# Kernel tuning notes

Measured on AMD Instinct MI355X. Metric: run time of the kernel, lower is better.

Reference implementation:

```python
import jax, jax.numpy as jnp
import numpy as np

DIM = 256
HEADS = 8
HD = DIM // HEADS  # 32
WS = 8             # window size
N = WS * WS        # 64 tokens per window
BN_SCALE = 1.0 / np.sqrt(1.0 + 1e-5)  # BatchNorm with default running stats (mean 0, var 1)


def _relative_position_index():
    # static int index table [N, N], computed with numpy (matches torch buffer)
    coords = np.stack(np.meshgrid(np.arange(WS), np.arange(WS), indexing='ij'))  # (2, ws, ws)
    cf = coords.reshape(2, -1)                                                   # (2, N)
    rel = cf[:, :, None] - cf[:, None, :]                                        # (2, N, N)
    rel = rel.transpose(1, 2, 0)                                                 # (N, N, 2)
    rel[:, :, 0] += WS - 1
    rel[:, :, 1] += WS - 1
    rel[:, :, 0] *= 2 * WS - 1
    return jnp.asarray(rel.sum(-1))  # (N, N)


def _relative_coords_table():
    # static float table [(2ws-1), (2ws-1), 2] with Swin-V2 log-spaced coords
    r = np.arange(-(WS - 1), WS, dtype=np.float32)
    g = np.stack(np.meshgrid(r, r, indexing='ij'), axis=-1)  # (L, L, 2)
    g = g / (WS - 1) * 8.0
    g = np.sign(g) * np.log2(np.abs(g) + 1.0) / np.log2(8.0)
    return jnp.asarray(g)


def setup_inputs() -> dict:
    key = jax.random.key(0)
    ks = jax.random.split(key, 9)
    B, H, W = 16, 64, 64
    s = 0.02
    return {
        'x': jax.random.normal(ks[0], (B, DIM, H, W), dtype=jnp.float32),
        'qkv_w': jax.random.normal(ks[1], (3 * DIM, DIM), dtype=jnp.float32) * s,
        'qkv_b': jax.random.normal(ks[2], (3 * DIM,), dtype=jnp.float32) * s,
        'proj_w': jax.random.normal(ks[3], (DIM, DIM), dtype=jnp.float32) * s,
        'proj_b': jax.random.normal(ks[4], (DIM,), dtype=jnp.float32) * s,
        'cpb_w1': jax.random.normal(ks[5], (DIM, 2), dtype=jnp.float32) * 0.5,
        'cpb_b1': jax.random.normal(ks[6], (DIM,), dtype=jnp.float32) * 0.5,
        'cpb_w2': jax.random.normal(ks[7], (HEADS, DIM), dtype=jnp.float32) * 0.1,
        'dw_w': jax.random.normal(ks[8], (DIM, 1, 7, 7), dtype=jnp.float32) * s,
    }


def reference(x, qkv_w, qkv_b, proj_w, proj_b, cpb_w1, cpb_b1, cpb_w2, dw_w):
    B, C, H, W = x.shape
    Hn, Wn = H // WS, W // WS
    B_ = B * Hn * Wn

    # continuous position bias: pointwise MLP (conv1x1+BN+SiLU, conv1x1+BN)
    tbl = _relative_coords_table()                          # (L, L, 2)
    h = jax.nn.silu((tbl @ cpb_w1.T + cpb_b1) * BN_SCALE)   # (L, L, DIM)
    bias_table = (h @ cpb_w2.T) * BN_SCALE                  # (L, L, HEADS)
    bias_table = bias_table.reshape(-1, HEADS)
    rpi = _relative_position_index()
    bias = bias_table[rpi.reshape(-1)].reshape(N, N, HEADS).transpose(2, 0, 1)
    bias = 16.0 * jax.nn.sigmoid(bias)                      # (HEADS, N, N)

    # qkv 1x1 conv, window partition
    qkv = jnp.einsum('oc,bchw->bohw', qkv_w, x) + qkv_b[None, :, None, None]
    win = qkv.reshape(B, 3 * C, Hn, WS, Wn, WS).transpose(0, 2, 4, 1, 3, 5)
    win = win.reshape(B_, 3 * C, N)
    qkvw = win.reshape(B_, 3, HEADS, HD, N).transpose(1, 0, 2, 4, 3)  # (3, B_, H, N, hd)
    q, k, v = qkvw[0], qkvw[1], qkvw[2]

    # SDPA with additive bias (attn_mask)
    scores = jnp.einsum('bhnd,bhmd->bhnm', q, k) / np.sqrt(HD) + bias[None]
    attn = jax.nn.softmax(scores, axis=-1)
    o = jnp.einsum('bhnm,bhmd->bhnd', attn, v)

    def window_reverse(w):  # (B_, N, C) -> (B, C, H, W)
        t = w.reshape(B, Hn, Wn, WS, WS, C).transpose(0, 5, 1, 3, 2, 4)
        return t.reshape(B, C, H, W)

    x_img = window_reverse(o.transpose(0, 2, 1, 3).reshape(B_, N, C))
    v_img = window_reverse(v.transpose(0, 2, 1, 3).reshape(B_, N, C))

    # depthwise 7x7 positional encoding on v, residual add
    pe = jax.lax.conv_general_dilated(
        v_img, dw_w, window_strides=(1, 1), padding='SAME',
        feature_group_count=C, dimension_numbers=('NCHW', 'OIHW', 'NCHW'))
    out = x_img + pe
    out = jnp.einsum('oc,bchw->bohw', proj_w, out) + proj_b[None, :, None, None]
    return out
```

## Files before the change

### kernel.cpp

```cpp
#include <hip/hip_runtime.h>
#include <cstdint>
#include <cstddef>

typedef unsigned short u16;
typedef unsigned int   u32;

#define LW     15
#define BNS    0.9999950000374997f
#define SCALE  0.17677669529663687f

typedef __bf16 bf16x8 __attribute__((ext_vector_type(8)));
typedef float  f32x4  __attribute__((ext_vector_type(4)));
typedef u16    u16x8  __attribute__((ext_vector_type(8)));

__device__ __forceinline__ u16 f2bf(float f){
  union { float f; u32 i; } v; v.f = f;
  u32 r = v.i + 0x7FFFu + ((v.i >> 16) & 1u);
  return (u16)(r >> 16);
}
__device__ __forceinline__ float bf2f(u16 u){
  union { u32 i; float f; } v; v.i = ((u32)u) << 16; return v.f;
}

__global__ void k_cvt_w(const float* __restrict__ qw, const float* __restrict__ pw,
                        u16* __restrict__ qwb, u16* __restrict__ pwb){
  const int i = blockIdx.x*256 + threadIdx.x;
  if (i < 196608) qwb[i] = f2bf(qw[i]);
  else            pwb[i - 196608] = f2bf(pw[i - 196608]);
}

__global__ void k_cpb_mlp(const float* __restrict__ w1, const float* __restrict__ b1,
                          const float* __restrict__ w2, float* __restrict__ tab){
  const int e = blockIdx.x;
  const int c = threadIdx.x;
  const float a0 = (float)(e / LW - 7);
  const float a1 = (float)(e % LW - 7);
  const float cx = copysignf(log2f(fabsf(a0)*(8.f/7.f) + 1.f) * (1.f/3.f), a0);
  const float cy = copysignf(log2f(fabsf(a1)*(8.f/7.f) + 1.f) * (1.f/3.f), a1);
  float pre = (cx*w1[2*c] + cy*w1[2*c+1] + b1[c]) * BNS;
  float hid = pre / (1.f + __expf(-pre));
  __shared__ float hl[256];
  hl[c] = hid;
  __syncthreads();
  if (c < 8){
    float s = 0.f;
    for (int i = 0; i < 256; ++i) s += hl[i] * w2[c*256 + i];
    tab[e*8 + c] = s * BNS;
  }
}

__global__ void k_bias_expand(const float* __restrict__ tab, float* __restrict__ biasQ){
  const int id = blockIdx.x*256 + threadIdx.x;
  const int key = id & 63;
  const int q   = (id >> 6) & 63;
  const int h   = id >> 12;
  const int dy = (q >> 3) - (key >> 3) + 7;
  const int dx = (q & 7)  - (key & 7)  + 7;
  const float v = tab[(dy*LW + dx)*8 + h];
  biasQ[id] = 16.f / (1.f + __expf(-v));
}

__global__ __launch_bounds__(512, 4) void k_qkv_attn(
    const float* __restrict__ x, const u16* __restrict__ qwb,
    const float* __restrict__ qb, const float* __restrict__ biasQ,
    float* __restrict__ xout, u16* __restrict__ vout){
  const int win = blockIdx.x;
  const int b = win >> 6, wy = (win >> 3) & 7, wx = win & 7;
  __shared__ __align__(16) char smem[70656];
  u16* xs = (u16*)smem;
  const int tid  = threadIdx.x;
  const int wave = tid >> 6, lane = tid & 63;
  const int quad = lane >> 4, l16 = lane & 15;
  u16* vbw = (u16*)(smem + 33792 + wave*4608);

  const float* xbase = x + (size_t)b*256*4096 + (size_t)(wy*8)*64 + wx*8;
  for (int i = tid; i < 4096; i += 512){
    const int c  = i >> 4;
    const int g  = i & 15;
    const int py = g >> 1, xh = (g & 1) * 4;
    float4 v4 = *(const float4*)&xbase[(size_t)c*4096 + py*64 + xh];
    const int n0 = py*8 + xh;
    xs[(n0+0)*264 + c] = f2bf(v4.x);
    xs[(n0+1)*264 + c] = f2bf(v4.y);
    xs[(n0+2)*264 + c] = f2bf(v4.z);
    xs[(n0+3)*264 + c] = f2bf(v4.w);
  }
  __syncthreads();

  const int h = wave;
  const f32x4 zero4 = {0.f, 0.f, 0.f, 0.f};

  auto run_gemm = [&](int sec, u32 (&w)[2][4][2]){
    f32x4 acc[2][4];
    #pragma unroll
    for (int rt = 0; rt < 2; ++rt)
      #pragma unroll
      for (int tt = 0; tt < 4; ++tt) acc[rt][tt] = zero4;
    #pragma unroll
    for (int kh2 = 0; kh2 < 2; ++kh2){
      bf16x8 af[2][4];
      #pragma unroll
      for (int rt = 0; rt < 2; ++rt){
        const int wr = sec*256 + h*32 + rt*16 + l16;
        #pragma unroll
        for (int kc = 0; kc < 4; ++kc)
          af[rt][kc] = *(const bf16x8*)(qwb + (size_t)wr*256 + (kh2*4 + kc)*32 + quad*8);
      }
      #pragma unroll
      for (int kc = 0; kc < 4; ++kc){
        #pragma unroll
        for (int tt = 0; tt < 4; ++tt){
          bf16x8 bf = *(const bf16x8*)&xs[(tt*16 + l16)*264 + (kh2*4 + kc)*32 + quad*8];
          acc[0][tt] = __builtin_amdgcn_mfma_f32_16x16x32_bf16(af[0][kc], bf, acc[0][tt], 0, 0, 0);
          acc[1][tt] = __builtin_amdgcn_mfma_f32_16x16x32_bf16(af[1][kc], bf, acc[1][tt], 0, 0, 0);
        }
      }
    }
    #pragma unroll
    for (int rt = 0; rt < 2; ++rt){
      float4 b4 = *(const float4*)&qb[sec*256 + h*32 + rt*16 + quad*4];
      #pragma unroll
      for (int tt = 0; tt < 4; ++tt){
        w[rt][tt][0] = (u32)f2bf(acc[rt][tt][0] + b4.x) |
                       ((u32)f2bf(acc[rt][tt][1] + b4.y) << 16);
        w[rt][tt][1] = (u32)f2bf(acc[rt][tt][2] + b4.z) |
                       ((u32)f2bf(acc[rt][tt][3] + b4.w) << 16);
      }
    }
  };

  auto bounce_td = [&](const u32 (&w)[2][4][2], bf16x8 (&frag)[4]){
    #pragma unroll
    for (int half = 0; half < 2; ++half){
      #pragma unroll
      for (int t2 = 0; t2 < 2; ++t2){
        const int tt = half*2 + t2;
        #pragma unroll
        for (int rt = 0; rt < 2; ++rt)
          #pragma unroll
          for (int u = 0; u < 2; ++u)
            *(u32*)&vbw[(t2*16 + l16)*40 + rt*16 + quad*4 + 2*u] = w[rt][tt][u];
      }
      #pragma unroll
      for (int t2 = 0; t2 < 2; ++t2)
        frag[half*2 + t2] = *(const bf16x8*)&vbw[(t2*16 + l16)*40 + quad*8];
    }
  };

  bf16x8 qf[4], ka[4];
  {
    u32 wq[2][4][2];
    run_gemm(0, wq);
    bounce_td(wq, qf);
  }
  {
    u32 wk[2][4][2];
    run_gemm(1, wk);
    bounce_td(wk, ka);
  }

  bf16x8 pa[4][2];
  #pragma unroll
  for (int qt = 0; qt < 4; ++qt){
    f32x4 st[4];
    #pragma unroll
    for (int kt = 0; kt < 4; ++kt)
      st[kt] = __builtin_amdgcn_mfma_f32_16x16x32_bf16(ka[kt], qf[qt], zero4, 0, 0, 0);
    float4 bq[4];
    #pragma unroll
    for (int kt = 0; kt < 4; ++kt)
      bq[kt] = *(const float4*)&biasQ[(h<<12) + (qt*16 + l16)*64 + kt*16 + quad*4];
    float sc[16], mx = -1e30f;
    #pragma unroll
    for (int kt = 0; kt < 4; ++kt)
      #pragma unroll
      for (int r = 0; r < 4; ++r){
        const float v = st[kt][r]*SCALE + ((const float*)&bq[kt])[r];
        sc[kt*4+r] = v; mx = fmaxf(mx, v);
      }
    mx = fmaxf(mx, __shfl_xor(mx, 16));
    mx = fmaxf(mx, __shfl_xor(mx, 32));
    float sum = 0.f;
    #pragma unroll
    for (int i = 0; i < 16; ++i){ sc[i] = __expf(sc[i] - mx); sum += sc[i]; }
    sum += __shfl_xor(sum, 16);
    sum += __shfl_xor(sum, 32);
    const float inv = 1.f / sum;
    #pragma unroll
    for (int kt = 0; kt < 4; ++kt){
      u32 w0 = (u32)f2bf(sc[kt*4+0]*inv) | ((u32)f2bf(sc[kt*4+1]*inv) << 16);
      u32 w1 = (u32)f2bf(sc[kt*4+2]*inv) | ((u32)f2bf(sc[kt*4+3]*inv) << 16);
      *(u32*)&vbw[l16*72 + kt*16 + quad*4 + 0] = w0;
      *(u32*)&vbw[l16*72 + kt*16 + quad*4 + 2] = w1;
    }
    pa[qt][0] = *(const bf16x8*)&vbw[l16*72 +  0 + quad*8];
    pa[qt][1] = *(const bf16x8*)&vbw[l16*72 + 32 + quad*8];
  }

  {
    u32 wv[2][4][2];
    run_gemm(2, wv);
    #pragma unroll
    for (int rt = 0; rt < 2; ++rt)
      #pragma unroll
      for (int tt = 0; tt < 4; ++tt)
        #pragma unroll
        for (int u = 0; u < 2; ++u){
          vbw[(rt*16 + quad*4 + 2*u + 0)*72 + tt*16 + l16] = (u16)(wv[rt][tt][u] & 0xFFFFu);
          vbw[(rt*16 + quad*4 + 2*u + 1)*72 + tt*16 + l16] = (u16)(wv[rt][tt][u] >> 16);
        }
  }
  bf16x8 bv[2][2];
  #pragma unroll
  for (int dt = 0; dt < 2; ++dt)
    #pragma unroll
    for (int kh = 0; kh < 2; ++kh)
      bv[dt][kh] = *(const bf16x8*)&vbw[(dt*16 + l16)*72 + kh*32 + quad*8];

  {
    const int d  = lane >> 1;
    #pragma unroll
    for (int i = 0; i < 4; ++i){
      const int ch = (lane & 1)*4 + i;
      u16x8 v8 = *(const u16x8*)&vbw[d*72 + ch*8];
      *(u16x8*)&vout[((size_t)(b*256 + h*32 + d))*4096 + (size_t)(wy*8 + ch)*64 + wx*8] = v8;
    }
  }

  #pragma unroll
  for (int qt = 0; qt < 4; ++qt){
    #pragma unroll
    for (int dt = 0; dt < 2; ++dt){
      f32x4 o = __builtin_amdgcn_mfma_f32_16x16x32_bf16(pa[qt][0], bv[dt][0], zero4, 0, 0, 0);
      o = __builtin_amdgcn_mfma_f32_16x16x32_bf16(pa[qt][1], bv[dt][1], o, 0, 0, 0);
      float4 o4; o4.x = o[0]; o4.y = o[1]; o4.z = o[2]; o4.w = o[3];
      *(float4*)&xout[((size_t)(b*256 + h*32 + dt*16 + l16))*4096
                      + (size_t)(wy*8 + qt*2 + (quad>>1))*64 + wx*8 + (quad&1)*4] = o4;
    }
  }
}

__global__ __launch_bounds__(256) void k_dwconv(
    const u16* __restrict__ vimg, const float* __restrict__ dww,
    float* __restrict__ io){
  const int b = blockIdx.x >> 8, c = blockIdx.x & 255;
  __shared__ float tile[70*72];
  const size_t base = ((size_t)(b*256 + c)) * 4096;
  for (int i = threadIdx.x; i < 1260; i += 256)
    *(float4*)&tile[i*4] = (float4){0.f, 0.f, 0.f, 0.f};
  float w[49];
  #pragma unroll
  for (int j = 0; j < 49; ++j) w[j] = dww[c*49 + j];
  __syncthreads();
  for (int i = threadIdx.x; i < 512; i += 256){
    const int y = i >> 3, x8 = (i & 7) * 8;
    u16x8 v = *(const u16x8*)&vimg[base + y*64 + x8];
    #pragma unroll
    for (int j = 0; j < 8; ++j) tile[(y+3)*72 + x8 + 3 + j] = bf2f(v[j]);
  }
  __syncthreads();

  const int x0 = (threadIdx.x & 15) * 4;
  const int y0 = (threadIdx.x >> 4) * 4;
  float acc[4][4];
  #pragma unroll
  for (int i = 0; i < 4; ++i)
    #pragma unroll
    for (int j = 0; j < 4; ++j) acc[i][j] = 0.f;

  #pragma unroll
  for (int ty = 0; ty < 10; ++ty){
    const float* rp = &tile[(y0 + ty)*72 + x0];
    float r[12];
    *(float4*)&r[0] = *(const float4*)&rp[0];
    *(float4*)&r[4] = *(const float4*)&rp[4];
    *(float4*)&r[8] = *(const float4*)&rp[8];
    #pragma unroll
    for (int oy = 0; oy < 4; ++oy){
      if (ty >= oy && ty - oy <= 6){
        const int ky = ty - oy;
        #pragma unroll
        for (int ox = 0; ox < 4; ++ox)
          #pragma unroll
          for (int kx = 0; kx < 7; ++kx)
            acc[oy][ox] += w[ky*7 + kx] * r[ox + kx];
      }
    }
  }
  #pragma unroll
  for (int oy = 0; oy < 4; ++oy){
    const size_t gi = base + (size_t)(y0 + oy)*64 + x0;
    float4 res = *(const float4*)&io[gi];
    res.x += acc[oy][0]; res.y += acc[oy][1];
    res.z += acc[oy][2]; res.w += acc[oy][3];
    *(float4*)&io[gi] = res;
  }
}

__global__ __launch_bounds__(256) void k_proj(
    const u16* __restrict__ pwb, const float* __restrict__ pb,
    float* __restrict__ io){
  const int row = blockIdx.x;
  const int b = row >> 6, y = row & 63;
  __shared__ __align__(16) u16 ts[64*264];
  const float* tbase = io + (size_t)b*256*4096 + (size_t)y*64;
  for (int i = threadIdx.x; i < 4096; i += 256){
    const int c = i >> 4, n0 = (i & 15) * 4;
    float4 v4 = *(const float4*)&tbase[(size_t)c*4096 + n0];
    ts[(n0+0)*264 + c] = f2bf(v4.x);
    ts[(n0+1)*264 + c] = f2bf(v4.y);
    ts[(n0+2)*264 + c] = f2bf(v4.z);
    ts[(n0+3)*264 + c] = f2bf(v4.w);
  }
  __syncthreads();
  const int wave = threadIdx.x >> 6, lane = threadIdx.x & 63;
  const int quad = lane >> 4, l16 = lane & 15;
  const f32x4 zero4 = {0.f, 0.f, 0.f, 0.f};
  #pragma unroll
  for (int op = 0; op < 2; ++op){
    bf16x8 af2[2][8];
    #pragma unroll
    for (int oj = 0; oj < 2; ++oj){
      const int orow = (wave*4 + op*2 + oj)*16 + l16;
      #pragma unroll
      for (int kc = 0; kc < 8; ++kc)
        af2[oj][kc] = *(const bf16x8*)(pwb + (size_t)orow*256 + kc*32 + quad*8);
    }
    f32x4 acc[2][4];
    #pragma unroll
    for (int oj = 0; oj < 2; ++oj)
      #pragma unroll
      for (int nt = 0; nt < 4; ++nt) acc[oj][nt] = zero4;
    #pragma unroll
    for (int kc = 0; kc < 8; ++kc){
      bf16x8 bf[4];
      #pragma unroll
      for (int nt = 0; nt < 4; ++nt)
        bf[nt] = *(const bf16x8*)&ts[(nt*16 + l16)*264 + kc*32 + quad*8];
      #pragma unroll
      for (int oj = 0; oj < 2; ++oj)
        #pragma unroll
        for (int nt = 0; nt < 4; ++nt)
          acc[oj][nt] = __builtin_amdgcn_mfma_f32_16x16x32_bf16(af2[oj][kc], bf[nt], acc[oj][nt], 0, 0, 0);
    }
    #pragma unroll
    for (int oj = 0; oj < 2; ++oj){
      const int ot = wave*4 + op*2 + oj;
      #pragma unroll
      for (int nt = 0; nt < 4; ++nt)
        #pragma unroll
        for (int r = 0; r < 4; ++r){
          const int o = ot*16 + quad*4 + r;
          io[((size_t)(b*256 + o))*4096 + (size_t)y*64 + nt*16 + l16] = acc[oj][nt][r] + pb[o];
        }
    }
  }
}

extern "C" void kernel_launch(void* const* d_in, const int* in_sizes, int n_in,
                              void* d_out, int out_size, void* d_ws, size_t ws_size,
                              hipStream_t stream){
  const float* x   = (const float*)d_in[0];
  const float* qw  = (const float*)d_in[1];
  const float* qb  = (const float*)d_in[2];
  const float* pw  = (const float*)d_in[3];
  const float* pb  = (const float*)d_in[4];
  const float* w1  = (const float*)d_in[5];
  const float* b1  = (const float*)d_in[6];
  const float* w2  = (const float*)d_in[7];
  const float* dww = (const float*)d_in[8];

  char* ws = (char*)d_ws;
  float* tab   = (float*)(ws);
  float* biasQ = (float*)(ws + 8192);
  u16*   qwb   = (u16*)  (ws + 139264);
  u16*   pwb   = (u16*)  (ws + 532480);
  u16*   vimg  = (u16*)  (ws + 663552);
  float* out   = (float*)d_out;

  k_cvt_w      <<<1024, 256, 0, stream>>>(qw, pw, qwb, pwb);
  k_cpb_mlp    <<<225,  256, 0, stream>>>(w1, b1, w2, tab);
  k_bias_expand<<<128,  256, 0, stream>>>(tab, biasQ);
  k_qkv_attn   <<<1024, 512, 0, stream>>>(x, qwb, qb, biasQ, out, vimg);
  k_dwconv     <<<4096, 256, 0, stream>>>(vimg, dww, out);
  k_proj       <<<1024, 256, 0, stream>>>(pwb, pb, out);
}
```

Before: 307.2 us.

## Fuse depthwise conv into projection kernel and shrink attention LDS scratch

Merges the depthwise 7x7 conv and the 1x1 projection into one kernel per image row. For each row it stages 7 rows of bf16 v across 32-channel groups in LDS, computes the conv plus the attention residual, and writes the bf16 result straight into the projection's transposed tile. This removes the fp32 read-modify-write round trip of the intermediate through global memory and one kernel launch. The attention kernel also halves its per-wave bounce buffer by staging one tile at a time, which cuts LDS from about 69KB to 51KB and may allow more resident blocks. In exchange, each v row is now read about 7 times across neighbouring blocks, and the conv work sits inside a larger-LDS, barrier-heavy loop that could lower occupancy.

```diff
diff --git a/kernel.cpp b/kernel.cpp
--- a/kernel.cpp
+++ b/kernel.cpp
@@ -66,12 +66,12 @@
     float* __restrict__ xout, u16* __restrict__ vout){
   const int win = blockIdx.x;
   const int b = win >> 6, wy = (win >> 3) & 7, wx = win & 7;
-  __shared__ __align__(16) char smem[70656];
+  __shared__ __align__(16) char smem[52224];
   u16* xs = (u16*)smem;
   const int tid  = threadIdx.x;
   const int wave = tid >> 6, lane = tid & 63;
   const int quad = lane >> 4, l16 = lane & 15;
-  u16* vbw = (u16*)(smem + 33792 + wave*4608);
+  u16* vbw = (u16*)(smem + 33792 + wave*2304);
 
   const float* xbase = x + (size_t)b*256*4096 + (size_t)(wy*8)*64 + wx*8;
   for (int i = tid; i < 4096; i += 512){
@@ -131,19 +131,13 @@
 
   auto bounce_td = [&](const u32 (&w)[2][4][2], bf16x8 (&frag)[4]){
     #pragma unroll
-    for (int half = 0; half < 2; ++half){
-      #pragma unroll
-      for (int t2 = 0; t2 < 2; ++t2){
-        const int tt = half*2 + t2;
-        #pragma unroll
-        for (int rt = 0; rt < 2; ++rt)
-          #pragma unroll
-          for (int u = 0; u < 2; ++u)
-            *(u32*)&vbw[(t2*16 + l16)*40 + rt*16 + quad*4 + 2*u] = w[rt][tt][u];
-      }
-      #pragma unroll
-      for (int t2 = 0; t2 < 2; ++t2)
-        frag[half*2 + t2] = *(const bf16x8*)&vbw[(t2*16 + l16)*40 + quad*8];
+    for (int tt = 0; tt < 4; ++tt){
+      #pragma unroll
+      for (int rt = 0; rt < 2; ++rt)
+        #pragma unroll
+        for (int u = 0; u < 2; ++u)
+          *(u32*)&vbw[l16*40 + rt*16 + quad*4 + 2*u] = w[rt][tt][u];
+      frag[tt] = *(const bf16x8*)&vbw[l16*40 + quad*8];
     }
   };
 
@@ -197,33 +191,30 @@
     pa[qt][1] = *(const bf16x8*)&vbw[l16*72 + 32 + quad*8];
   }
 
+  bf16x8 bv[2][2];
   {
     u32 wv[2][4][2];
     run_gemm(2, wv);
     #pragma unroll
-    for (int rt = 0; rt < 2; ++rt)
+    for (int rt = 0; rt < 2; ++rt){
       #pragma unroll
       for (int tt = 0; tt < 4; ++tt)
         #pragma unroll
         for (int u = 0; u < 2; ++u){
-          vbw[(rt*16 + quad*4 + 2*u + 0)*72 + tt*16 + l16] = (u16)(wv[rt][tt][u] & 0xFFFFu);
-          vbw[(rt*16 + quad*4 + 2*u + 1)*72 + tt*16 + l16] = (u16)(wv[rt][tt][u] >> 16);
+          vbw[(quad*4 + 2*u + 0)*72 + tt*16 + l16] = (u16)(wv[rt][tt][u] & 0xFFFFu);
+          vbw[(quad*4 + 2*u + 1)*72 + tt*16 + l16] = (u16)(wv[rt][tt][u] >> 16);
         }
-  }
-  bf16x8 bv[2][2];
-  #pragma unroll
-  for (int dt = 0; dt < 2; ++dt)
-    #pragma unroll
-    for (int kh = 0; kh < 2; ++kh)
-      bv[dt][kh] = *(const bf16x8*)&vbw[(dt*16 + l16)*72 + kh*32 + quad*8];
-
-  {
-    const int d  = lane >> 1;
-    #pragma unroll
-    for (int i = 0; i < 4; ++i){
-      const int ch = (lane & 1)*4 + i;
-      u16x8 v8 = *(const u16x8*)&vbw[d*72 + ch*8];
-      *(u16x8*)&vout[((size_t)(b*256 + h*32 + d))*4096 + (size_t)(wy*8 + ch)*64 + wx*8] = v8;
+      #pragma unroll
+      for (int kh = 0; kh < 2; ++kh)
+        bv[rt][kh] = *(const bf16x8*)&vbw[l16*72 + kh*32 + quad*8];
+      const int dl = lane >> 2;
+      #pragma unroll
+      for (int j = 0; j < 2; ++j){
+        const int ch = (lane & 3)*2 + j;
+        u16x8 v8 = *(const u16x8*)&vbw[dl*72 + ch*8];
+        *(u16x8*)&vout[((size_t)(b*256 + h*32 + rt*16 + dl))*4096
+                       + (size_t)(wy*8 + ch)*64 + wx*8] = v8;
+      }
     }
   }
 
@@ -240,80 +231,88 @@
   }
 }
 
-__global__ __launch_bounds__(256) void k_dwconv(
+__global__ __launch_bounds__(256) void k_dwproj(
     const u16* __restrict__ vimg, const float* __restrict__ dww,
-    float* __restrict__ io){
-  const int b = blockIdx.x >> 8, c = blockIdx.x & 255;
-  __shared__ float tile[70*72];
-  const size_t base = ((size_t)(b*256 + c)) * 4096;
-  for (int i = threadIdx.x; i < 1260; i += 256)
-    *(float4*)&tile[i*4] = (float4){0.f, 0.f, 0.f, 0.f};
-  float w[49];
-  #pragma unroll
-  for (int j = 0; j < 49; ++j) w[j] = dww[c*49 + j];
-  __syncthreads();
-  for (int i = threadIdx.x; i < 512; i += 256){
-    const int y = i >> 3, x8 = (i & 7) * 8;
-    u16x8 v = *(const u16x8*)&vimg[base + y*64 + x8];
-    #pragma unroll
-    for (int j = 0; j < 8; ++j) tile[(y+3)*72 + x8 + 3 + j] = bf2f(v[j]);
-  }
-  __syncthreads();
-
-  const int x0 = (threadIdx.x & 15) * 4;
-  const int y0 = (threadIdx.x >> 4) * 4;
-  float acc[4][4];
-  #pragma unroll
-  for (int i = 0; i < 4; ++i)
-    #pragma unroll
-    for (int j = 0; j < 4; ++j) acc[i][j] = 0.f;
-
-  #pragma unroll
-  for (int ty = 0; ty < 10; ++ty){
-    const float* rp = &tile[(y0 + ty)*72 + x0];
-    float r[12];
-    *(float4*)&r[0] = *(const float4*)&rp[0];
-    *(float4*)&r[4] = *(const float4*)&rp[4];
-    *(float4*)&r[8] = *(const float4*)&rp[8];
-    #pragma unroll
-    for (int oy = 0; oy < 4; ++oy){
-      if (ty >= oy && ty - oy <= 6){
-        const int ky = ty - oy;
-        #pragma unroll
-        for (int ox = 0; ox < 4; ++ox)
-          #pragma unroll
-          for (int kx = 0; kx < 7; ++kx)
-            acc[oy][ox] += w[ky*7 + kx] * r[ox + kx];
-      }
-    }
-  }
-  #pragma unroll
-  for (int oy = 0; oy < 4; ++oy){
-    const size_t gi = base + (size_t)(y0 + oy)*64 + x0;
-    float4 res = *(const float4*)&io[gi];
-    res.x += acc[oy][0]; res.y += acc[oy][1];
-    res.z += acc[oy][2]; res.w += acc[oy][3];
-    *(float4*)&io[gi] = res;
-  }
-}
-
-__global__ __launch_bounds__(256) void k_proj(
     const u16* __restrict__ pwb, const float* __restrict__ pb,
     float* __restrict__ io){
   const int row = blockIdx.x;
   const int b = row >> 6, y = row & 63;
-  __shared__ __align__(16) u16 ts[64*264];
-  const float* tbase = io + (size_t)b*256*4096 + (size_t)y*64;
-  for (int i = threadIdx.x; i < 4096; i += 256){
-    const int c = i >> 4, n0 = (i & 15) * 4;
-    float4 v4 = *(const float4*)&tbase[(size_t)c*4096 + n0];
-    ts[(n0+0)*264 + c] = f2bf(v4.x);
-    ts[(n0+1)*264 + c] = f2bf(v4.y);
-    ts[(n0+2)*264 + c] = f2bf(v4.z);
-    ts[(n0+3)*264 + c] = f2bf(v4.w);
-  }
+  __shared__ __align__(16) char smem[81536];
+  u16*   vs = (u16*)(smem);
+  float* rb = (float*)(smem + 32256);
+  float* wl = (float*)(smem + 41472);
+  u16*   ts = (u16*)(smem + 47744);
+  const int tid = threadIdx.x;
+
+  for (int i = tid; i < 2016; i += 256)
+    *(float4*)&vs[i*8] = (float4){0.f, 0.f, 0.f, 0.f};
   __syncthreads();
-  const int wave = threadIdx.x >> 6, lane = threadIdx.x & 63;
+
+  const size_t iobase = (size_t)b*256*4096 + (size_t)y*64;
+
+  for (int e = 0; e < 8; ++e){
+    const int cg = e*32;
+    for (int i = tid; i < 1792; i += 256){
+      const int x8 = i & 7, ch = (i >> 3) & 31, dyi = i >> 8;
+      const int ry = y + dyi - 3;
+      u16x8 v8 = {0,0,0,0,0,0,0,0};
+      if (ry >= 0 && ry < 64)
+        v8 = *(const u16x8*)&vimg[((size_t)(b*256 + cg + ch))*4096 + ry*64 + x8*8];
+      u16* dst = &vs[ch*504 + dyi*72 + 4 + x8*8];
+      *(ushort4*)&dst[0] = (ushort4){v8[0], v8[1], v8[2], v8[3]};
+      *(ushort4*)&dst[4] = (ushort4){v8[4], v8[5], v8[6], v8[7]};
+    }
+    for (int i = tid; i < 512; i += 256){
+      const int ch = i >> 4, x4 = i & 15;
+      float4 f4 = *(const float4*)&io[iobase + (size_t)(cg + ch)*4096 + x4*4];
+      *(float4*)&rb[ch*72 + x4*4] = f4;
+    }
+    for (int i = tid; i < 392; i += 256){
+      float4 f4 = *(const float4*)&dww[cg*49 + i*4];
+      *(float4*)&wl[i*4] = f4;
+    }
+    __syncthreads();
+
+    {
+      const int ch = tid & 31, x0 = (tid >> 5) * 8;
+      float w[49];
+      #pragma unroll
+      for (int j = 0; j < 49; ++j) w[j] = wl[ch*49 + j];
+      float acc[8];
+      #pragma unroll
+      for (int i = 0; i < 8; ++i) acc[i] = 0.f;
+      #pragma unroll
+      for (int dy = 0; dy < 7; ++dy){
+        const u16* vp = &vs[ch*504 + dy*72 + x0];
+        float r[16];
+        #pragma unroll
+        for (int k = 0; k < 8; ++k){
+          u32 pr = *(const u32*)&vp[2*k];
+          r[2*k]   = bf2f((u16)(pr & 0xFFFFu));
+          r[2*k+1] = bf2f((u16)(pr >> 16));
+        }
+        #pragma unroll
+        for (int dx = 0; dx < 7; ++dx)
+          #pragma unroll
+          for (int i = 0; i < 8; ++i)
+            acc[i] += w[dy*7 + dx] * r[i + dx + 1];
+      }
+      float4 i0 = *(const float4*)&rb[ch*72 + x0];
+      float4 i1 = *(const float4*)&rb[ch*72 + x0 + 4];
+      const int c = cg + ch;
+      ts[(x0+0)*264 + c] = f2bf(acc[0] + i0.x);
+      ts[(x0+1)*264 + c] = f2bf(acc[1] + i0.y);
+      ts[(x0+2)*264 + c] = f2bf(acc[2] + i0.z);
+      ts[(x0+3)*264 + c] = f2bf(acc[3] + i0.w);
+      ts[(x0+4)*264 + c] = f2bf(acc[4] + i1.x);
+      ts[(x0+5)*264 + c] = f2bf(acc[5] + i1.y);
+      ts[(x0+6)*264 + c] = f2bf(acc[6] + i1.z);
+      ts[(x0+7)*264 + c] = f2bf(acc[7] + i1.w);
+    }
+    __syncthreads();
+  }
+
+  const int wave = tid >> 6, lane = tid & 63;
   const int quad = lane >> 4, l16 = lane & 15;
   const f32x4 zero4 = {0.f, 0.f, 0.f, 0.f};
   #pragma unroll
@@ -382,6 +381,5 @@
   k_cpb_mlp    <<<225,  256, 0, stream>>>(w1, b1, w2, tab);
   k_bias_expand<<<128,  256, 0, stream>>>(tab, biasQ);
   k_qkv_attn   <<<1024, 512, 0, stream>>>(x, qwb, qb, biasQ, out, vimg);
-  k_dwconv     <<<4096, 256, 0, stream>>>(vimg, dww, out);
-  k_proj       <<<1024, 256, 0, stream>>>(pwb, pb, out);
-}
+  k_dwproj     <<<1024, 256, 0, stream>>>(vimg, dww, pwb, pb, out);
+}
```

After: 344.3 us. 12.1% more time.

## Store conv+attn sum as bf16 and halve attention V staging LDS

Applied to the files above, without the earlier changes.

The depthwise conv kernel now writes the sum of the attention output and the positional-encoding conv as bf16 into the V image buffer, instead of read-modify-writing fp32 in place. The projection kernel then loads bf16 directly rather than fp32 followed by a conversion. This removes one fp32 write pass and halves the projection's input read. The attention kernel also stages the V tile in two 16-row halves, cutting per-wave LDS to shrink the block's shared-memory footprint. Precision is unchanged, because the projection already rounded its input to bf16.

```diff
diff --git a/kernel.cpp b/kernel.cpp
--- a/kernel.cpp
+++ b/kernel.cpp
@@ -66,12 +66,12 @@
     float* __restrict__ xout, u16* __restrict__ vout){
   const int win = blockIdx.x;
   const int b = win >> 6, wy = (win >> 3) & 7, wx = win & 7;
-  __shared__ __align__(16) char smem[70656];
+  __shared__ __align__(16) char smem[54272];
   u16* xs = (u16*)smem;
   const int tid  = threadIdx.x;
   const int wave = tid >> 6, lane = tid & 63;
   const int quad = lane >> 4, l16 = lane & 15;
-  u16* vbw = (u16*)(smem + 33792 + wave*4608);
+  u16* vbw = (u16*)(smem + 33792 + wave*2560);
 
   const float* xbase = x + (size_t)b*256*4096 + (size_t)(wy*8)*64 + wx*8;
   for (int i = tid; i < 4096; i += 512){
@@ -197,33 +197,30 @@
     pa[qt][1] = *(const bf16x8*)&vbw[l16*72 + 32 + quad*8];
   }
 
+  bf16x8 bv[2][2];
   {
     u32 wv[2][4][2];
     run_gemm(2, wv);
     #pragma unroll
-    for (int rt = 0; rt < 2; ++rt)
+    for (int rt = 0; rt < 2; ++rt){
       #pragma unroll
       for (int tt = 0; tt < 4; ++tt)
         #pragma unroll
         for (int u = 0; u < 2; ++u){
-          vbw[(rt*16 + quad*4 + 2*u + 0)*72 + tt*16 + l16] = (u16)(wv[rt][tt][u] & 0xFFFFu);
-          vbw[(rt*16 + quad*4 + 2*u + 1)*72 + tt*16 + l16] = (u16)(wv[rt][tt][u] >> 16);
+          vbw[(quad*4 + 2*u + 0)*72 + tt*16 + l16] = (u16)(wv[rt][tt][u] & 0xFFFFu);
+          vbw[(quad*4 + 2*u + 1)*72 + tt*16 + l16] = (u16)(wv[rt][tt][u] >> 16);
         }
-  }
-  bf16x8 bv[2][2];
-  #pragma unroll
-  for (int dt = 0; dt < 2; ++dt)
-    #pragma unroll
-    for (int kh = 0; kh < 2; ++kh)
-      bv[dt][kh] = *(const bf16x8*)&vbw[(dt*16 + l16)*72 + kh*32 + quad*8];
-
-  {
-    const int d  = lane >> 1;
-    #pragma unroll
-    for (int i = 0; i < 4; ++i){
-      const int ch = (lane & 1)*4 + i;
-      u16x8 v8 = *(const u16x8*)&vbw[d*72 + ch*8];
-      *(u16x8*)&vout[((size_t)(b*256 + h*32 + d))*4096 + (size_t)(wy*8 + ch)*64 + wx*8] = v8;
+      #pragma unroll
+      for (int kh = 0; kh < 2; ++kh)
+        bv[rt][kh] = *(const bf16x8*)&vbw[l16*72 + kh*32 + quad*8];
+      const int dl = lane >> 2;
+      #pragma unroll
+      for (int j = 0; j < 2; ++j){
+        const int ch = (lane & 3)*2 + j;
+        u16x8 v8 = *(const u16x8*)&vbw[dl*72 + ch*8];
+        *(u16x8*)&vout[((size_t)(b*256 + h*32 + rt*16 + dl))*4096
+                       + (size_t)(wy*8 + ch)*64 + wx*8] = v8;
+      }
     }
   }
 
@@ -241,8 +238,8 @@
 }
 
 __global__ __launch_bounds__(256) void k_dwconv(
-    const u16* __restrict__ vimg, const float* __restrict__ dww,
-    float* __restrict__ io){
+    const float* __restrict__ io, const float* __restrict__ dww,
+    u16* __restrict__ vimg){
   const int b = blockIdx.x >> 8, c = blockIdx.x & 255;
   __shared__ float tile[70*72];
   const size_t base = ((size_t)(b*256 + c)) * 4096;
@@ -291,26 +288,27 @@
   for (int oy = 0; oy < 4; ++oy){
     const size_t gi = base + (size_t)(y0 + oy)*64 + x0;
     float4 res = *(const float4*)&io[gi];
-    res.x += acc[oy][0]; res.y += acc[oy][1];
-    res.z += acc[oy][2]; res.w += acc[oy][3];
-    *(float4*)&io[gi] = res;
+    ushort4 pk;
+    pk.x = f2bf(res.x + acc[oy][0]);
+    pk.y = f2bf(res.y + acc[oy][1]);
+    pk.z = f2bf(res.z + acc[oy][2]);
+    pk.w = f2bf(res.w + acc[oy][3]);
+    *(ushort4*)&vimg[gi] = pk;
   }
 }
 
 __global__ __launch_bounds__(256) void k_proj(
     const u16* __restrict__ pwb, const float* __restrict__ pb,
-    float* __restrict__ io){
+    const u16* __restrict__ vimg, float* __restrict__ io){
   const int row = blockIdx.x;
   const int b = row >> 6, y = row & 63;
   __shared__ __align__(16) u16 ts[64*264];
-  const float* tbase = io + (size_t)b*256*4096 + (size_t)y*64;
-  for (int i = threadIdx.x; i < 4096; i += 256){
-    const int c = i >> 4, n0 = (i & 15) * 4;
-    float4 v4 = *(const float4*)&tbase[(size_t)c*4096 + n0];
-    ts[(n0+0)*264 + c] = f2bf(v4.x);
-    ts[(n0+1)*264 + c] = f2bf(v4.y);
-    ts[(n0+2)*264 + c] = f2bf(v4.z);
-    ts[(n0+3)*264 + c] = f2bf(v4.w);
+  const u16* tbase = vimg + (size_t)b*256*4096 + (size_t)y*64;
+  for (int i = threadIdx.x; i < 2048; i += 256){
+    const int c = i >> 3, x8 = (i & 7) * 8;
+    u16x8 v = *(const u16x8*)&tbase[(size_t)c*4096 + x8];
+    #pragma unroll
+    for (int j = 0; j < 8; ++j) ts[(x8+j)*264 + c] = v[j];
   }
   __syncthreads();
   const int wave = threadIdx.x >> 6, lane = threadIdx.x & 63;
@@ -382,6 +380,6 @@
   k_cpb_mlp    <<<225,  256, 0, stream>>>(w1, b1, w2, tab);
   k_bias_expand<<<128,  256, 0, stream>>>(tab, biasQ);
   k_qkv_attn   <<<1024, 512, 0, stream>>>(x, qwb, qb, biasQ, out, vimg);
-  k_dwconv     <<<4096, 256, 0, stream>>>(vimg, dww, out);
-  k_proj       <<<1024, 256, 0, stream>>>(pwb, pb, out);
-}
+  k_dwconv     <<<4096, 256, 0, stream>>>(out, dww, vimg);
+  k_proj       <<<1024, 256, 0, stream>>>(pwb, pb, vimg, out);
+}
```

Result: no change. 310.1 us (+0.9%).

## Store attention intermediates in window-major layout and pass dwconv result as bf16

Applied to the files above, without the earlier changes.

The attention kernel now writes its output and V in a per-window contiguous layout instead of image NCHW. The dwconv kernel reads from that layout, adds the conv to the attention output, and writes the sum as bf16 into the V buffer in place, which k_proj then reads directly. This halves the traffic into the projection and removes the fp32 read-modify-write of the output. The Q weight fragments are also preloaded into registers before the x tile load, and the launch bound is relaxed to 2 blocks per CU. That extra register use may lower occupancy, and the in-place overwrite of V relies on each dwconv block touching only its own channel.

```diff
diff --git a/kernel.cpp b/kernel.cpp
--- a/kernel.cpp
+++ b/kernel.cpp
@@ -60,10 +60,10 @@
   biasQ[id] = 16.f / (1.f + __expf(-v));
 }
 
-__global__ __launch_bounds__(512, 4) void k_qkv_attn(
+__global__ __launch_bounds__(512, 2) void k_qkv_attn(
     const float* __restrict__ x, const u16* __restrict__ qwb,
     const float* __restrict__ qb, const float* __restrict__ biasQ,
-    float* __restrict__ xout, u16* __restrict__ vout){
+    float* __restrict__ ow, u16* __restrict__ vw){
   const int win = blockIdx.x;
   const int b = win >> 6, wy = (win >> 3) & 7, wx = win & 7;
   __shared__ __align__(16) char smem[70656];
@@ -72,6 +72,16 @@
   const int wave = tid >> 6, lane = tid & 63;
   const int quad = lane >> 4, l16 = lane & 15;
   u16* vbw = (u16*)(smem + 33792 + wave*4608);
+  const int h = wave;
+
+  bf16x8 afq[2][8];
+  #pragma unroll
+  for (int rt = 0; rt < 2; ++rt){
+    const int wr = h*32 + rt*16 + l16;
+    #pragma unroll
+    for (int kc = 0; kc < 8; ++kc)
+      afq[rt][kc] = *(const bf16x8*)(qwb + (size_t)wr*256 + kc*32 + quad*8);
+  }
 
   const float* xbase = x + (size_t)b*256*4096 + (size_t)(wy*8)*64 + wx*8;
   for (int i = tid; i < 4096; i += 512){
@@ -87,8 +97,35 @@
   }
   __syncthreads();
 
-  const int h = wave;
   const f32x4 zero4 = {0.f, 0.f, 0.f, 0.f};
+
+  auto run_gemm_pre = [&](const bf16x8 (&af)[2][8], int sec, u32 (&w)[2][4][2]){
+    f32x4 acc[2][4];
+    #pragma unroll
+    for (int rt = 0; rt < 2; ++rt)
+      #pragma unroll
+      for (int tt = 0; tt < 4; ++tt) acc[rt][tt] = zero4;
+    #pragma unroll
+    for (int kc = 0; kc < 8; ++kc){
+      #pragma unroll
+      for (int tt = 0; tt < 4; ++tt){
+        bf16x8 bf = *(const bf16x8*)&xs[(tt*16 + l16)*264 + kc*32 + quad*8];
+        acc[0][tt] = __builtin_amdgcn_mfma_f32_16x16x32_bf16(af[0][kc], bf, acc[0][tt], 0, 0, 0);
+        acc[1][tt] = __builtin_amdgcn_mfma_f32_16x16x32_bf16(af[1][kc], bf, acc[1][tt], 0, 0, 0);
+      }
+    }
+    #pragma unroll
+    for (int rt = 0; rt < 2; ++rt){
+      float4 b4 = *(const float4*)&qb[sec*256 + h*32 + rt*16 + quad*4];
+      #pragma unroll
+      for (int tt = 0; tt < 4; ++tt){
+        w[rt][tt][0] = (u32)f2bf(acc[rt][tt][0] + b4.x) |
+                       ((u32)f2bf(acc[rt][tt][1] + b4.y) << 16);
+        w[rt][tt][1] = (u32)f2bf(acc[rt][tt][2] + b4.z) |
+                       ((u32)f2bf(acc[rt][tt][3] + b4.w) << 16);
+      }
+    }
+  };
 
   auto run_gemm = [&](int sec, u32 (&w)[2][4][2]){
     f32x4 acc[2][4];
@@ -150,7 +187,7 @@
   bf16x8 qf[4], ka[4];
   {
     u32 wq[2][4][2];
-    run_gemm(0, wq);
+    run_gemm_pre(afq, 0, wq);
     bounce_td(wq, qf);
   }
   {
@@ -218,12 +255,12 @@
       bv[dt][kh] = *(const bf16x8*)&vbw[(dt*16 + l16)*72 + kh*32 + quad*8];
 
   {
-    const int d  = lane >> 1;
+    const int d = lane >> 1;
     #pragma unroll
     for (int i = 0; i < 4; ++i){
       const int ch = (lane & 1)*4 + i;
       u16x8 v8 = *(const u16x8*)&vbw[d*72 + ch*8];
-      *(u16x8*)&vout[((size_t)(b*256 + h*32 + d))*4096 + (size_t)(wy*8 + ch)*64 + wx*8] = v8;
+      *(u16x8*)&vw[(size_t)win*16384 + (h*32 + d)*64 + ch*8] = v8;
     }
   }
 
@@ -234,18 +271,17 @@
       f32x4 o = __builtin_amdgcn_mfma_f32_16x16x32_bf16(pa[qt][0], bv[dt][0], zero4, 0, 0, 0);
       o = __builtin_amdgcn_mfma_f32_16x16x32_bf16(pa[qt][1], bv[dt][1], o, 0, 0, 0);
       float4 o4; o4.x = o[0]; o4.y = o[1]; o4.z = o[2]; o4.w = o[3];
-      *(float4*)&xout[((size_t)(b*256 + h*32 + dt*16 + l16))*4096
-                      + (size_t)(wy*8 + qt*2 + (quad>>1))*64 + wx*8 + (quad&1)*4] = o4;
+      *(float4*)&ow[(size_t)win*16384 + (h*32 + dt*16 + l16)*64 + qt*16 + quad*4] = o4;
     }
   }
 }
 
 __global__ __launch_bounds__(256) void k_dwconv(
-    const u16* __restrict__ vimg, const float* __restrict__ dww,
-    float* __restrict__ io){
+    const float* __restrict__ ow, const float* __restrict__ dww,
+    u16* __restrict__ vw){
   const int b = blockIdx.x >> 8, c = blockIdx.x & 255;
   __shared__ float tile[70*72];
-  const size_t base = ((size_t)(b*256 + c)) * 4096;
+  const size_t wb = (size_t)b*64*16384 + (size_t)c*64;
   for (int i = threadIdx.x; i < 1260; i += 256)
     *(float4*)&tile[i*4] = (float4){0.f, 0.f, 0.f, 0.f};
   float w[49];
@@ -253,10 +289,12 @@
   for (int j = 0; j < 49; ++j) w[j] = dww[c*49 + j];
   __syncthreads();
   for (int i = threadIdx.x; i < 512; i += 256){
-    const int y = i >> 3, x8 = (i & 7) * 8;
-    u16x8 v = *(const u16x8*)&vimg[base + y*64 + x8];
-    #pragma unroll
-    for (int j = 0; j < 8; ++j) tile[(y+3)*72 + x8 + 3 + j] = bf2f(v[j]);
+    const int win = i >> 3, py = i & 7;
+    u16x8 v = *(const u16x8*)&vw[wb + (size_t)win*16384 + py*8];
+    const int y = ((win >> 3) << 3) + py, xw = (win & 7)*8;
+    float* dst = &tile[(y+3)*72 + xw + 3];
+    #pragma unroll
+    for (int j = 0; j < 8; ++j) dst[j] = bf2f(v[j]);
   }
   __syncthreads();
 
@@ -287,30 +325,36 @@
       }
     }
   }
+  const int winx = x0 >> 3;
   #pragma unroll
   for (int oy = 0; oy < 4; ++oy){
-    const size_t gi = base + (size_t)(y0 + oy)*64 + x0;
-    float4 res = *(const float4*)&io[gi];
-    res.x += acc[oy][0]; res.y += acc[oy][1];
-    res.z += acc[oy][2]; res.w += acc[oy][3];
-    *(float4*)&io[gi] = res;
+    const int y   = y0 + oy;
+    const int win = ((y >> 3) << 3) + winx;
+    const int n0  = (y & 7)*8 + (x0 & 7);
+    const size_t off = wb + (size_t)win*16384 + n0;
+    float4 res = *(const float4*)&ow[off];
+    ushort4 pk;
+    pk.x = f2bf(res.x + acc[oy][0]);
+    pk.y = f2bf(res.y + acc[oy][1]);
+    pk.z = f2bf(res.z + acc[oy][2]);
+    pk.w = f2bf(res.w + acc[oy][3]);
+    *(ushort4*)&vw[off] = pk;
   }
 }
 
 __global__ __launch_bounds__(256) void k_proj(
     const u16* __restrict__ pwb, const float* __restrict__ pb,
-    float* __restrict__ io){
+    const u16* __restrict__ vw, float* __restrict__ io){
   const int row = blockIdx.x;
   const int b = row >> 6, y = row & 63;
+  const int wy = y >> 3, py = y & 7;
   __shared__ __align__(16) u16 ts[64*264];
-  const float* tbase = io + (size_t)b*256*4096 + (size_t)y*64;
-  for (int i = threadIdx.x; i < 4096; i += 256){
-    const int c = i >> 4, n0 = (i & 15) * 4;
-    float4 v4 = *(const float4*)&tbase[(size_t)c*4096 + n0];
-    ts[(n0+0)*264 + c] = f2bf(v4.x);
-    ts[(n0+1)*264 + c] = f2bf(v4.y);
-    ts[(n0+2)*264 + c] = f2bf(v4.z);
-    ts[(n0+3)*264 + c] = f2bf(v4.w);
+  for (int i = threadIdx.x; i < 2048; i += 256){
+    const int c = i >> 3, g = i & 7;
+    u16x8 v = *(const u16x8*)&vw[((size_t)(b*64 + wy*8 + g))*16384 + c*64 + py*8];
+    const int x8 = g*8;
+    #pragma unroll
+    for (int j = 0; j < 8; ++j) ts[(x8+j)*264 + c] = v[j];
   }
   __syncthreads();
   const int wave = threadIdx.x >> 6, lane = threadIdx.x & 63;
@@ -375,13 +419,13 @@
   float* biasQ = (float*)(ws + 8192);
   u16*   qwb   = (u16*)  (ws + 139264);
   u16*   pwb   = (u16*)  (ws + 532480);
-  u16*   vimg  = (u16*)  (ws + 663552);
+  u16*   vw    = (u16*)  (ws + 663552);
   float* out   = (float*)d_out;
 
   k_cvt_w      <<<1024, 256, 0, stream>>>(qw, pw, qwb, pwb);
   k_cpb_mlp    <<<225,  256, 0, stream>>>(w1, b1, w2, tab);
   k_bias_expand<<<128,  256, 0, stream>>>(tab, biasQ);
-  k_qkv_attn   <<<1024, 512, 0, stream>>>(x, qwb, qb, biasQ, out, vimg);
-  k_dwconv     <<<4096, 256, 0, stream>>>(vimg, dww, out);
-  k_proj       <<<1024, 256, 0, stream>>>(pwb, pb, out);
-}
+  k_qkv_attn   <<<1024, 512, 0, stream>>>(x, qwb, qb, biasQ, out, vw);
+  k_dwconv     <<<4096, 256, 0, stream>>>(out, dww, vw);
+  k_proj       <<<1024, 256, 0, stream>>>(pwb, pb, vw, out);
+}
```

Measured after the change: 305.1 us. No clear change (-0.7%).
